# Kernel tuning notes

Hardware: AMD Instinct MI355X
Metric: run time of the kernel (lower is better)

Reference implementation:

```python
import jax, jax.numpy as jnp
import numpy as np

SCALE = 1.0  # from init_kwargs scale=1

def setup_inputs() -> dict:
    key = jax.random.key(0)
    x = jax.random.normal(key, (8192, 8192), dtype=jnp.float32)  # [B, S]
    return {"x": x}

def reference(x) -> jnp.ndarray:
    # mtx_diff @ x[:, :, None]: first-difference along seq, with element 0 forced to 0
    # (mtx_diff[0,0] = 0 in the original).
    d = x[:, 1:] - x[:, :-1]                      # [B, S-1]
    d = jnp.concatenate([jnp.zeros_like(x[:, :1]), d], axis=1)  # [B, S]
    t = jnp.tanh(d / SCALE)
    # mtx_sum (lower-triangular ones incl. diagonal) @ t: inclusive cumulative sum.
    return jnp.cumsum(t, axis=1)                  # [B, S]
```

## Files before the change

### kernel.cpp

```cpp
#include <hip/hip_runtime.h>

#define ROW  8192
#define NT   256
#define NW   (NT / 64)
#define G    8

__device__ __forceinline__ float fast_tanh(float d) {
    float e = __expf(2.0f * d);
    return 1.0f - 2.0f * __builtin_amdgcn_rcpf(e + 1.0f);
}

__global__ __launch_bounds__(NT) void diff_tanh_cumsum(const float* __restrict__ x,
                                                       float* __restrict__ out) {
    __shared__ float tot[NW * G];

    const int t    = threadIdx.x;
    const int lane = t & 63;
    const int w    = t >> 6;
    const long long rb = (long long)blockIdx.x * ROW;

    float4 v[G];
    #pragma unroll
    for (int g = 0; g < G; ++g)
        v[g] = *reinterpret_cast<const float4*>(x + rb + (t + NT * g) * 4);

    float4 p[G];
    float  s[G];
    #pragma unroll
    for (int g = 0; g < G; ++g) {
        const int i0 = (t + NT * g) * 4;
        float prev = __shfl_up(v[g].w, 1, 64);
        if (lane == 0) prev = (i0 > 0) ? x[rb + i0 - 1] : v[g].x;
        float t0 = fast_tanh(v[g].x - prev);
        float t1 = fast_tanh(v[g].y - v[g].x);
        float t2 = fast_tanh(v[g].z - v[g].y);
        float t3 = fast_tanh(v[g].w - v[g].z);
        float q0 = t0;
        float q1 = q0 + t1;
        float q2 = q1 + t2;
        float q3 = q2 + t3;
        p[g] = make_float4(q0, q1, q2, q3);
        s[g] = q3;
    }

    float ws[G];
    #pragma unroll
    for (int g = 0; g < G; ++g) ws[g] = s[g];
    #pragma unroll
    for (int d = 1; d < 64; d <<= 1) {
        #pragma unroll
        for (int g = 0; g < G; ++g) {
            float o = __shfl_up(ws[g], d, 64);
            if (lane >= d) ws[g] += o;
        }
    }

    if (lane == 63) {
        #pragma unroll
        for (int g = 0; g < G; ++g) tot[w * G + g] = ws[g];
    }
    __syncthreads();

    float run = 0.0f;
    float off[G];
    #pragma unroll
    for (int g = 0; g < G; ++g) {
        float wpre = 0.0f, gtot = 0.0f;
        #pragma unroll
        for (int ww = 0; ww < NW; ++ww) {
            float tv = tot[ww * G + g];
            gtot += tv;
            if (ww < w) wpre += tv;
        }
        off[g] = run + wpre + (ws[g] - s[g]);
        run += gtot;
    }

    #pragma unroll
    for (int g = 0; g < G; ++g) {
        float4 o;
        o.x = p[g].x + off[g];
        o.y = p[g].y + off[g];
        o.z = p[g].z + off[g];
        o.w = p[g].w + off[g];
        *reinterpret_cast<float4*>(out + rb + (t + NT * g) * 4) = o;
    }
}

extern "C" void kernel_launch(void* const* d_in, const int* in_sizes, int n_in,
                              void* d_out, int out_size, void* d_ws, size_t ws_size,
                              hipStream_t stream) {
    const float* x = (const float*)d_in[0];
    float* out = (float*)d_out;
    const int rows = in_sizes[0] / ROW;
    diff_tanh_cumsum<<<rows, NT, 0, stream>>>(x, out);
}
```

Measured before the change: 109.5 us.

## Double block width, share chunk boundaries via LDS, use nontemporal stores

Moves to 512 threads per block with 4 float4 chunks per thread instead of 256 threads with 8, so each thread holds half as much in registers and each block has more waves. Boundary values between wave chunks now come from a shared-memory table instead of extra scalar global loads, at the cost of an additional __syncthreads. Prefix results are written back into the input vector registers, and outputs go out with nontemporal stores so the streaming writes do not pollute the cache.

```diff
diff --git a/kernel.cpp b/kernel.cpp
--- a/kernel.cpp
+++ b/kernel.cpp
@@ -1,9 +1,11 @@
 #include <hip/hip_runtime.h>
 
 #define ROW  8192
-#define NT   256
+#define NT   512
 #define NW   (NT / 64)
-#define G    8
+#define G    4
+
+typedef float f32x4 __attribute__((ext_vector_type(4)));
 
 __device__ __forceinline__ float fast_tanh(float d) {
     float e = __expf(2.0f * d);
@@ -12,35 +14,43 @@
 
 __global__ __launch_bounds__(NT) void diff_tanh_cumsum(const float* __restrict__ x,
                                                        float* __restrict__ out) {
-    __shared__ float tot[NW * G];
+    __shared__ float last[NW][G];
+    __shared__ float tot[NW][G];
 
     const int t    = threadIdx.x;
     const int lane = t & 63;
     const int w    = t >> 6;
     const long long rb = (long long)blockIdx.x * ROW;
 
-    float4 v[G];
+    f32x4 v[G];
     #pragma unroll
     for (int g = 0; g < G; ++g)
-        v[g] = *reinterpret_cast<const float4*>(x + rb + (t + NT * g) * 4);
+        v[g] = *reinterpret_cast<const f32x4*>(x + rb + (t + NT * g) * 4);
 
-    float4 p[G];
-    float  s[G];
+    if (lane == 63) {
+        #pragma unroll
+        for (int g = 0; g < G; ++g) last[w][g] = v[g].w;
+    }
+    __syncthreads();
+
+    float s[G];
     #pragma unroll
     for (int g = 0; g < G; ++g) {
-        const int i0 = (t + NT * g) * 4;
         float prev = __shfl_up(v[g].w, 1, 64);
-        if (lane == 0) prev = (i0 > 0) ? x[rb + i0 - 1] : v[g].x;
+        if (lane == 0) {
+            prev = (w > 0) ? last[w - 1][g]
+                 : (g > 0) ? last[NW - 1][g - 1]
+                           : v[g].x;
+        }
         float t0 = fast_tanh(v[g].x - prev);
         float t1 = fast_tanh(v[g].y - v[g].x);
         float t2 = fast_tanh(v[g].z - v[g].y);
         float t3 = fast_tanh(v[g].w - v[g].z);
-        float q0 = t0;
-        float q1 = q0 + t1;
-        float q2 = q1 + t2;
-        float q3 = q2 + t3;
-        p[g] = make_float4(q0, q1, q2, q3);
-        s[g] = q3;
+        v[g].x = t0;
+        v[g].y = v[g].x + t1;
+        v[g].z = v[g].y + t2;
+        v[g].w = v[g].z + t3;
+        s[g]   = v[g].w;
     }
 
     float ws[G];
@@ -57,7 +67,7 @@
 
     if (lane == 63) {
         #pragma unroll
-        for (int g = 0; g < G; ++g) tot[w * G + g] = ws[g];
+        for (int g = 0; g < G; ++g) tot[w][g] = ws[g];
     }
     __syncthreads();
 
@@ -68,7 +78,7 @@
         float wpre = 0.0f, gtot = 0.0f;
         #pragma unroll
         for (int ww = 0; ww < NW; ++ww) {
-            float tv = tot[ww * G + g];
+            float tv = tot[ww][g];
             gtot += tv;
             if (ww < w) wpre += tv;
         }
@@ -78,12 +88,12 @@
 
     #pragma unroll
     for (int g = 0; g < G; ++g) {
-        float4 o;
-        o.x = p[g].x + off[g];
-        o.y = p[g].y + off[g];
-        o.z = p[g].z + off[g];
-        o.w = p[g].w + off[g];
-        *reinterpret_cast<float4*>(out + rb + (t + NT * g) * 4) = o;
+        f32x4 o;
+        o.x = v[g].x + off[g];
+        o.y = v[g].y + off[g];
+        o.z = v[g].z + off[g];
+        o.w = v[g].w + off[g];
+        __builtin_nontemporal_store(o, reinterpret_cast<f32x4*>(out + rb + (t + NT * g) * 4));
     }
 }
 
```

After: 87.62 us. 1.25x faster.
